# Performance work log

Hardware: AMD Instinct MI355X
Metric: run time of the kernel (lower is better)

The kernel has to match this reference:

```python
import jax, jax.numpy as jnp
import numpy as np
from jax import lax

B, NK, NQ, DK, DV, H = 4, 4096, 4096, 64, 64, 256


def _linear_params(key, fan_in, fan_out):
    kw, kb = jax.random.split(key)
    lim = 1.0 / np.sqrt(fan_in)
    w = jax.random.uniform(kw, (fan_out, fan_in), jnp.float32, -lim, lim)
    b = jax.random.uniform(kb, (fan_out,), jnp.float32, -lim, lim)
    return w, b


def setup_inputs() -> dict:
    key = jax.random.key(0)
    ks = jax.random.split(key, 9)
    inp = {
        "KEY": jax.random.normal(ks[0], (B, NK, DK), jnp.float32),
        "VALUE": jax.random.normal(ks[1], (B, NK, DV), jnp.float32),
        "QUERY": jax.random.normal(ks[2], (B, NQ, DK), jnp.float32),
    }
    inp["W1_w"], inp["W1_b"] = _linear_params(ks[3], DK, H)
    inp["W2_w"], inp["W2_b"] = _linear_params(ks[4], H, H)
    inp["W3_w"], inp["W3_b"] = _linear_params(ks[5], H, DK)
    inp["Wo1_w"], inp["Wo1_b"] = _linear_params(ks[6], DK, H)
    inp["Wo2_w"], inp["Wo2_b"] = _linear_params(ks[7], H, H)
    inp["Wo3_w"], inp["Wo3_b"] = _linear_params(ks[8], H, DV)
    return inp


def _mlp(x, w1, b1, w2, b2, w3, b3):
    h = jax.nn.relu(jnp.einsum('bnd,hd->bnh', x, w1) + b1)
    h = jax.nn.relu(jnp.einsum('bnh,gh->bng', h, w2) + b2)
    return jnp.einsum('bng,og->bno', h, w3) + b3


def _l1_cdist(K, Q):
    # K: [b,nk,d], Q: [b,nq,d] -> [b,nk,nq]; scan over feature dim to avoid
    # materializing the [b,nk,nq,d] difference tensor.
    b, nk, _ = K.shape
    nq = Q.shape[1]

    def body(acc, kq):
        k, q = kq  # [b,nk], [b,nq]
        return acc + jnp.abs(k[:, :, None] - q[:, None, :]), None

    init = jnp.zeros((b, nk, nq), K.dtype)
    score, _ = lax.scan(body, init, (jnp.moveaxis(K, -1, 0), jnp.moveaxis(Q, -1, 0)))
    return score


def reference(KEY, VALUE, QUERY, W1_w, W1_b, W2_w, W2_b, W3_w, W3_b,
              Wo1_w, Wo1_b, Wo2_w, Wo2_b, Wo3_w, Wo3_b):
    Wk = _mlp(KEY, W1_w, W1_b, W2_w, W2_b, W3_w, W3_b)
    Wq = _mlp(QUERY, W1_w, W1_b, W2_w, W2_b, W3_w, W3_b)
    Wo = _mlp(QUERY, Wo1_w, Wo1_b, Wo2_w, Wo2_b, Wo3_w, Wo3_b)
    KEY_scale = KEY * Wk          # [b,nk,dk]
    QUERY_scale = QUERY * Wq      # [b,nq,dk]
    score = _l1_cdist(KEY_scale, QUERY_scale)            # [b,nk,nq]
    attn = jax.nn.softmax(-(score * score) * 0.5, axis=1)  # softmax over keys
    context = jnp.einsum('bik,bij->bkj', attn, VALUE)    # [b,nq,dv]
    # dropout is identity in eval mode
    return context * Wo
```

## Files before the change

kernel.cpp:

```cpp
#include <hip/hip_runtime.h>
#include <hip/hip_bf16.h>
#include <stdint.h>

#define B_DIM 4
#define NKK 4096
#define NQQ 4096
#define DD 64
#define HH 256

typedef __attribute__((ext_vector_type(4))) float floatx4;
typedef __attribute__((ext_vector_type(2))) float floatx2;
typedef __attribute__((ext_vector_type(8))) short bf16x8;

__device__ __forceinline__ float fexp2(float x) { return __builtin_amdgcn_exp2f(x); }
__device__ __forceinline__ unsigned fbits(float x) { return __float_as_uint(x); }
__device__ __forceinline__ float bf2f(unsigned short u) { return __uint_as_float(((unsigned)u) << 16); }

__device__ __forceinline__ floatx2 pk_sub(floatx2 a, floatx2 b) {
  floatx2 d;
  asm("v_pk_add_f32 %0, %1, %2 neg_lo:[0,1] neg_hi:[0,1]" : "=v"(d) : "v"(a), "v"(b));
  return d;
}

__device__ __forceinline__ void splitbf(float x, unsigned short& h, unsigned short& l) {
  unsigned u = fbits(x);
  unsigned hu = (u + 0x7fff + ((u >> 16) & 1)) & 0xffff0000u;
  h = (unsigned short)(hu >> 16);
  l = (unsigned short)(fbits(x - __uint_as_float(hu)) >> 16);
}

#define FSTRIDE 68
#define FSTRIDE4 17

__global__ __launch_bounds__(256) void wsplit_kernel(
    const float* __restrict__ W1a, const float* __restrict__ W2a, const float* __restrict__ W3a,
    const float* __restrict__ W1b, const float* __restrict__ W2b, const float* __restrict__ W3b,
    unsigned short* __restrict__ sp)
{
  int idx = blockIdx.x * 256 + threadIdx.x;
  const int set = idx >= 98304;
  int r = idx - set * 98304;
  unsigned short* base = sp + (size_t)set * 196608;
  const float* src;
  unsigned short *dh, *dl;
  int j;
  if (r < 16384)      { src = set ? W1b : W1a; dh = base;          dl = base + 16384;  j = r; }
  else if (r < 81920) { src = set ? W2b : W2a; dh = base + 32768;  dl = base + 98304;  j = r - 16384; }
  else                { src = set ? W3b : W3a; dh = base + 163840; dl = base + 180224; j = r - 81920; }
  unsigned short h, l;
  splitbf(src[j], h, l);
  dh[j] = h; dl[j] = l;
}

__global__ __launch_bounds__(256) void vtrans_kernel(
    const float* __restrict__ V, unsigned short* __restrict__ Vt)
{
  __shared__ unsigned short t[64][80];
  const int tid = threadIdx.x;
  const int b = blockIdx.y;
  const int k0 = blockIdx.x * 64;
  const float4* V4 = (const float4*)V;
  {
    const int r = tid & 63;
    const int c4 = tid >> 6;
#pragma unroll
    for (int j = 0; j < 4; ++j) {
      float4 f = V4[((size_t)(b * NKK + k0 + r)) * 16 + c4 * 4 + j];
      const int d0 = c4 * 16 + j * 4;
      t[d0 + 0][r] = (unsigned short)(fbits(f.x) >> 16);
      t[d0 + 1][r] = (unsigned short)(fbits(f.y) >> 16);
      t[d0 + 2][r] = (unsigned short)(fbits(f.z) >> 16);
      t[d0 + 3][r] = (unsigned short)(fbits(f.w) >> 16);
    }
  }
  __syncthreads();
  {
    const int d = tid >> 2;
    const int kc = tid & 3;
    uint4 u0 = *(const uint4*)&t[d][kc * 16];
    uint4 u1 = *(const uint4*)&t[d][kc * 16 + 8];
    unsigned short* dst = Vt + ((size_t)(b * 64 + d)) * NKK + k0 + kc * 16;
    *(uint4*)dst = u0;
    *(uint4*)(dst + 8) = u1;
  }
}

#define HSTRIDE 264
__global__ __launch_bounds__(512, 1) void mlpmm_kernel(
    const float* __restrict__ KEY, const float* __restrict__ QUERY,
    const float* __restrict__ B1a, const float* __restrict__ B2a, const float* __restrict__ B3a,
    const float* __restrict__ B1b, const float* __restrict__ B2b, const float* __restrict__ B3b,
    const unsigned short* __restrict__ sp,
    float* __restrict__ Ks, float* __restrict__ Qs, float* __restrict__ Wo)
{
  __shared__ unsigned short Xh[64][72], Xl[64][72];
  __shared__ unsigned short Hsh[64][HSTRIDE], Hsl[64][HSTRIDE];
  const int tid = threadIdx.x;
  const int w = tid >> 6;
  const int lane = tid & 63;
  const int l15 = lane & 15;
  const int quad = lane >> 4;

  const int g = blockIdx.x;
  const float* X;
  float* outp;
  int mulx, t0;
  const unsigned short* wb;
  const float *b1, *b2, *b3;
  if (g < 256)      { X = KEY;   outp = Ks; mulx = 1; t0 = g * 64;         wb = sp;          b1 = B1a; b2 = B2a; b3 = B3a; }
  else if (g < 512) { X = QUERY; outp = Qs; mulx = 1; t0 = (g - 256) * 64; wb = sp;          b1 = B1a; b2 = B2a; b3 = B3a; }
  else              { X = QUERY; outp = Wo; mulx = 0; t0 = (g - 512) * 64; wb = sp + 196608; b1 = B1b; b2 = B2b; b3 = B3b; }
  const unsigned short* W1h = wb;
  const unsigned short* W1l = wb + 16384;
  const unsigned short* W2h = wb + 32768;
  const unsigned short* W2l = wb + 98304;
  const unsigned short* W3h = wb + 163840;
  const unsigned short* W3l = wb + 180224;

  {
    const int t = tid >> 3;
    const int c = (tid & 7) * 8;
    float4 a = *(const float4*)&X[(size_t)(t0 + t) * 64 + c];
    float4 b = *(const float4*)&X[(size_t)(t0 + t) * 64 + c + 4];
    float v[8] = {a.x, a.y, a.z, a.w, b.x, b.y, b.z, b.w};
    unsigned short hs[8], ls[8];
#pragma unroll
    for (int e = 0; e < 8; ++e) splitbf(v[e], hs[e], ls[e]);
    uint4 uh = make_uint4(hs[0] | ((unsigned)hs[1] << 16), hs[2] | ((unsigned)hs[3] << 16),
                          hs[4] | ((unsigned)hs[5] << 16), hs[6] | ((unsigned)hs[7] << 16));
    uint4 ul = make_uint4(ls[0] | ((unsigned)ls[1] << 16), ls[2] | ((unsigned)ls[3] << 16),
                          ls[4] | ((unsigned)ls[5] << 16), ls[6] | ((unsigned)ls[7] << 16));
    *(uint4*)&Xh[t][c] = uh;
    *(uint4*)&Xl[t][c] = ul;
  }
  __syncthreads();

  {
    floatx4 acc[4][2];
#pragma unroll
    for (int nb = 0; nb < 2; ++nb) {
      const float bias = b1[(w * 2 + nb) * 16 + l15];
#pragma unroll
      for (int mb = 0; mb < 4; ++mb) acc[mb][nb] = (floatx4){bias, bias, bias, bias};
    }
#pragma unroll
    for (int kb = 0; kb < 2; ++kb) {
      bf16x8 Ah[4], Al[4];
#pragma unroll
      for (int mb = 0; mb < 4; ++mb) {
        Ah[mb] = *(const bf16x8*)&Xh[mb * 16 + l15][kb * 32 + quad * 8];
        Al[mb] = *(const bf16x8*)&Xl[mb * 16 + l15][kb * 32 + quad * 8];
      }
#pragma unroll
      for (int nb = 0; nb < 2; ++nb) {
        const int n0 = (w * 2 + nb) * 16;
        bf16x8 Bh = *(const bf16x8*)&W1h[(size_t)(n0 + l15) * 64 + kb * 32 + quad * 8];
        bf16x8 Bl = *(const bf16x8*)&W1l[(size_t)(n0 + l15) * 64 + kb * 32 + quad * 8];
#pragma unroll
        for (int mb = 0; mb < 4; ++mb) {
          acc[mb][nb] = __builtin_amdgcn_mfma_f32_16x16x32_bf16(Ah[mb], Bh, acc[mb][nb], 0, 0, 0);
          acc[mb][nb] = __builtin_amdgcn_mfma_f32_16x16x32_bf16(Al[mb], Bh, acc[mb][nb], 0, 0, 0);
          acc[mb][nb] = __builtin_amdgcn_mfma_f32_16x16x32_bf16(Ah[mb], Bl, acc[mb][nb], 0, 0, 0);
        }
      }
    }
#pragma unroll
    for (int mb = 0; mb < 4; ++mb)
#pragma unroll
      for (int nb = 0; nb < 2; ++nb) {
        const int col = (w * 2 + nb) * 16 + l15;
#pragma unroll
        for (int r = 0; r < 4; ++r) {
          const int row = mb * 16 + quad * 4 + r;
          float v = fmaxf(acc[mb][nb][r], 0.0f);
          unsigned short h, l;
          splitbf(v, h, l);
          Hsh[row][col] = h;
          Hsl[row][col] = l;
        }
      }
  }
  __syncthreads();

  {
    floatx4 acc2[4][2];
#pragma unroll
    for (int nb = 0; nb < 2; ++nb) {
      const float bias = b2[(w * 2 + nb) * 16 + l15];
#pragma unroll
      for (int mb = 0; mb < 4; ++mb) acc2[mb][nb] = (floatx4){bias, bias, bias, bias};
    }
#pragma unroll
    for (int kb = 0; kb < 8; ++kb) {
      bf16x8 Ah[4], Al[4];
#pragma unroll
      for (int mb = 0; mb < 4; ++mb) {
        Ah[mb] = *(const bf16x8*)&Hsh[mb * 16 + l15][kb * 32 + quad * 8];
        Al[mb] = *(const bf16x8*)&Hsl[mb * 16 + l15][kb * 32 + quad * 8];
      }
#pragma unroll
      for (int nb = 0; nb < 2; ++nb) {
        const int n0 = (w * 2 + nb) * 16;
        bf16x8 Bh = *(const bf16x8*)&W2h[(size_t)(n0 + l15) * 256 + kb * 32 + quad * 8];
        bf16x8 Bl = *(const bf16x8*)&W2l[(size_t)(n0 + l15) * 256 + kb * 32 + quad * 8];
#pragma unroll
        for (int mb = 0; mb < 4; ++mb) {
          acc2[mb][nb] = __builtin_amdgcn_mfma_f32_16x16x32_bf16(Ah[mb], Bh, acc2[mb][nb], 0, 0, 0);
          acc2[mb][nb] = __builtin_amdgcn_mfma_f32_16x16x32_bf16(Al[mb], Bh, acc2[mb][nb], 0, 0, 0);
          acc2[mb][nb] = __builtin_amdgcn_mfma_f32_16x16x32_bf16(Ah[mb], Bl, acc2[mb][nb], 0, 0, 0);
        }
      }
    }
    __syncthreads();
#pragma unroll
    for (int mb = 0; mb < 4; ++mb)
#pragma unroll
      for (int nb = 0; nb < 2; ++nb) {
        const int col = (w * 2 + nb) * 16 + l15;
#pragma unroll
        for (int r = 0; r < 4; ++r) {
          const int row = mb * 16 + quad * 4 + r;
          float v = fmaxf(acc2[mb][nb][r], 0.0f);
          unsigned short h, l;
          splitbf(v, h, l);
          Hsh[row][col] = h;
          Hsl[row][col] = l;
        }
      }
  }
  __syncthreads();

  {
    const int mp = (w >> 2) * 2;
    const int n0 = (w & 3) * 16;
    const float bias = b3[n0 + l15];
    floatx4 acc3[2];
#pragma unroll
    for (int m = 0; m < 2; ++m) acc3[m] = (floatx4){bias, bias, bias, bias};
#pragma unroll
    for (int kb = 0; kb < 8; ++kb) {
      bf16x8 Ah[2], Al[2];
#pragma unroll
      for (int m = 0; m < 2; ++m) {
        Ah[m] = *(const bf16x8*)&Hsh[(mp + m) * 16 + l15][kb * 32 + quad * 8];
        Al[m] = *(const bf16x8*)&Hsl[(mp + m) * 16 + l15][kb * 32 + quad * 8];
      }
      bf16x8 Bh = *(const bf16x8*)&W3h[(size_t)(n0 + l15) * 256 + kb * 32 + quad * 8];
      bf16x8 Bl = *(const bf16x8*)&W3l[(size_t)(n0 + l15) * 256 + kb * 32 + quad * 8];
#pragma unroll
      for (int m = 0; m < 2; ++m) {
        acc3[m] = __builtin_amdgcn_mfma_f32_16x16x32_bf16(Ah[m], Bh, acc3[m], 0, 0, 0);
        acc3[m] = __builtin_amdgcn_mfma_f32_16x16x32_bf16(Al[m], Bh, acc3[m], 0, 0, 0);
        acc3[m] = __builtin_amdgcn_mfma_f32_16x16x32_bf16(Ah[m], Bl, acc3[m], 0, 0, 0);
      }
    }
#pragma unroll
    for (int m = 0; m < 2; ++m)
#pragma unroll
      for (int r = 0; r < 4; ++r) {
        const int row = (mp + m) * 16 + quad * 4 + r;
        const int col = n0 + l15;
        float v = acc3[m][r];
        if (mulx) v *= (bf2f(Xh[row][col]) + bf2f(Xl[row][col]));
        outp[(size_t)(t0 + row) * 64 + col] = v;
      }
  }
}

template <int ITERS, bool PARTIAL>
__global__ __launch_bounds__(256, 3) void attn_kernel(
    const float* __restrict__ Ksg, const float* __restrict__ Qsg,
    const unsigned short* __restrict__ Vtg, const float* __restrict__ Wog,
    float* __restrict__ outp,
    float* __restrict__ Pm, float* __restrict__ Pl, float* __restrict__ PO)
{
  __shared__ float qsA[32 * FSTRIDE];
  __shared__ float ksA[4][32 * FSTRIDE];
  __shared__ unsigned short psB[4][32 * 40];
  __shared__ float abA[4][32];

  const int tid  = threadIdx.x;
  const int w    = tid >> 6;
  const int lane = tid & 63;
  const int lq   = lane >> 3;
  const int lk   = lane & 7;
  const int l15  = lane & 15;
  const int quad = lane >> 4;
  const int b    = blockIdx.y;
  const int qt   = blockIdx.x * 32;

  {
    const int row = tid >> 3;
    const int c0  = (tid & 7) * 2;
    const float4* Q4 = (const float4*)Qsg;
    float4 g0 = Q4[(size_t)(b * NQQ + qt + row) * 16 + c0];
    float4 g1 = Q4[(size_t)(b * NQQ + qt + row) * 16 + c0 + 1];
    *(float4*)&qsA[row * FSTRIDE + c0 * 4]     = g0;
    *(float4*)&qsA[row * FSTRIDE + c0 * 4 + 4] = g1;
  }
  __syncthreads();

  float m_i[4], l_i[4];
  floatx4 acc[2][4];
#pragma unroll
  for (int i = 0; i < 4; ++i) { m_i[i] = -3.0e38f; l_i[i] = 0.0f; }
#pragma unroll
  for (int mb = 0; mb < 2; ++mb)
#pragma unroll
    for (int nb = 0; nb < 4; ++nb)
#pragma unroll
      for (int r = 0; r < 4; ++r) acc[mb][nb][r] = 0.0f;

  const int kstart = (blockIdx.z * 4 + w) * (ITERS * 32);
  const float4* K4 = (const float4*)Ksg;
  const float NEG_HALF_LOG2E = -0.72134752044448170f;

  const int krow = (lane >> 4);
  const int kci  = lane & 15;

  const unsigned short* vg0 = Vtg + ((size_t)b * 64 + l15) * NKK + kstart + quad * 8;

  float4 kpre[8];
  uint4 vtpre[4];
#pragma unroll
  for (int c = 0; c < 8; ++c)
    kpre[c] = K4[(size_t)(b * NKK + kstart + c * 4 + krow) * 16 + kci];
#pragma unroll
  for (int nb = 0; nb < 4; ++nb)
    vtpre[nb] = *(const uint4*)(vg0 + (size_t)nb * 16 * NKK);

  const floatx4* qb = (const floatx4*)&qsA[lq * FSTRIDE];
  const floatx4* kb = (const floatx4*)&ksA[w][lk * FSTRIDE];

  for (int it = 0; it < ITERS; ++it) {
#pragma unroll
    for (int c = 0; c < 8; ++c)
      *(float4*)&ksA[w][(c * 4 + krow) * FSTRIDE + kci * 4] = kpre[c];

    {
      const int itn = (it + 1 < ITERS) ? it + 1 : it;
#pragma unroll
      for (int c = 0; c < 8; ++c)
        kpre[c] = K4[(size_t)(b * NKK + kstart + itn * 32 + c * 4 + krow) * 16 + kci];
    }

    float s[4][4];
#pragma unroll
    for (int i = 0; i < 4; ++i)
#pragma unroll
      for (int j = 0; j < 4; ++j) s[i][j] = 0.0f;

#pragma unroll
    for (int dc = 0; dc < 16; ++dc) {
      floatx4 qv[4], kv[4];
#pragma unroll
      for (int i = 0; i < 4; ++i) qv[i] = qb[i * (8 * FSTRIDE4) + dc];
#pragma unroll
      for (int j = 0; j < 4; ++j) kv[j] = kb[j * (8 * FSTRIDE4) + dc];
#pragma unroll
      for (int i = 0; i < 4; ++i) {
        const floatx2 qlo = qv[i].lo, qhi = qv[i].hi;
#pragma unroll
        for (int j = 0; j < 4; ++j) {
          floatx2 d0 = pk_sub(qlo, kv[j].lo);
          floatx2 d1 = pk_sub(qhi, kv[j].hi);
          s[i][j] += __builtin_fabsf(d0.x);
          s[i][j] += __builtin_fabsf(d0.y);
          s[i][j] += __builtin_fabsf(d1.x);
          s[i][j] += __builtin_fabsf(d1.y);
        }
      }
    }

    float a_row[4];
#pragma unroll
    for (int i = 0; i < 4; ++i) {
      float smin = fminf(fminf(s[i][0], s[i][1]), fminf(s[i][2], s[i][3]));
      smin = fminf(smin, __shfl_xor(smin, 1));
      smin = fminf(smin, __shfl_xor(smin, 2));
      smin = fminf(smin, __shfl_xor(smin, 4));
      const float tmax = smin * smin * NEG_HALF_LOG2E;
      const float mn = fmaxf(m_i[i], tmax);
      a_row[i] = fexp2(m_i[i] - mn);
      m_i[i] = mn;
      float ps = 0.0f;
#pragma unroll
      for (int j = 0; j < 4; ++j) {
        const float sv = s[i][j];
        const float e = fexp2(fmaf(sv * NEG_HALF_LOG2E, sv, -mn));
        ps += e;
        psB[w][(lq + 8 * i) * 40 + lk + 8 * j] = (unsigned short)(fbits(e) >> 16);
      }
      l_i[i] = fmaf(l_i[i], a_row[i], ps);
    }
    if (lk == 0) {
#pragma unroll
      for (int i = 0; i < 4; ++i) abA[w][lq + 8 * i] = a_row[i];
    }

    {
      bf16x8 afrag[2];
#pragma unroll
      for (int mb = 0; mb < 2; ++mb)
        afrag[mb] = *(const bf16x8*)&psB[w][(mb * 16 + l15) * 40 + quad * 8];

      const floatx4 arv0 = *(const floatx4*)&abA[w][quad * 4];
      const floatx4 arv1 = *(const floatx4*)&abA[w][16 + quad * 4];

#pragma unroll
      for (int nb = 0; nb < 4; ++nb) {
        bf16x8 bfrag = __builtin_bit_cast(bf16x8, vtpre[nb]);
        acc[0][nb] *= arv0;
        acc[1][nb] *= arv1;
        acc[0][nb] = __builtin_amdgcn_mfma_f32_16x16x32_bf16(afrag[0], bfrag, acc[0][nb], 0, 0, 0);
        acc[1][nb] = __builtin_amdgcn_mfma_f32_16x16x32_bf16(afrag[1], bfrag, acc[1][nb], 0, 0, 0);
      }
    }

    {
      const int itn = (it + 1 < ITERS) ? it + 1 : it;
#pragma unroll
      for (int nb = 0; nb < 4; ++nb)
        vtpre[nb] = *(const uint4*)(vg0 + (size_t)nb * 16 * NKK + itn * 32);
    }
  }

#pragma unroll
  for (int i = 0; i < 4; ++i) {
    float l = l_i[i];
    l += __shfl_xor(l, 1);
    l += __shfl_xor(l, 2);
    l += __shfl_xor(l, 4);
    l_i[i] = l;
  }
  float* ovl = (float*)&psB[w][0];
  if (lk == 0) {
#pragma unroll
    for (int i = 0; i < 4; ++i) {
      ovl[lq + 8 * i]      = m_i[i];
      ovl[32 + lq + 8 * i] = l_i[i];
    }
  }
#pragma unroll
  for (int mb = 0; mb < 2; ++mb)
#pragma unroll
    for (int nb = 0; nb < 4; ++nb)
#pragma unroll
      for (int r = 0; r < 4; ++r)
        ksA[w][(mb * 16 + quad * 4 + r) * 64 + nb * 16 + l15] = acc[mb][nb][r];
  __syncthreads();

  {
    const int q = tid >> 3;
    const int dbase = (tid & 7) * 8;
    const float m0 = ((const float*)&psB[0][0])[q];
    const float m1 = ((const float*)&psB[1][0])[q];
    const float m2 = ((const float*)&psB[2][0])[q];
    const float m3 = ((const float*)&psB[3][0])[q];
    const float M = fmaxf(fmaxf(m0, m1), fmaxf(m2, m3));
    const float s0 = fexp2(m0 - M), s1 = fexp2(m1 - M);
    const float s2v = fexp2(m2 - M), s3 = fexp2(m3 - M);
    const float L = ((const float*)&psB[0][0])[32 + q] * s0 +
                    ((const float*)&psB[1][0])[32 + q] * s1 +
                    ((const float*)&psB[2][0])[32 + q] * s2v +
                    ((const float*)&psB[3][0])[32 + q] * s3;
    if (PARTIAL) {
      const size_t p = (size_t)(blockIdx.z * 4 + b) * 128 + blockIdx.x;
      if (dbase == 0) { Pm[p * 32 + q] = M; Pl[p * 32 + q] = L; }
      float* dst = PO + p * 2048 + q * 64 + dbase;
#pragma unroll
      for (int c = 0; c < 8; ++c) {
        const int d = dbase + c;
        dst[c] = s0 * ksA[0][q * 64 + d] + s1 * ksA[1][q * 64 + d] +
                 s2v * ksA[2][q * 64 + d] + s3 * ksA[3][q * 64 + d];
      }
    } else {
      const float rL = 1.0f / L;
      const size_t gbase = (size_t)(b * NQQ + qt + q) * 64 + dbase;
#pragma unroll
      for (int c = 0; c < 8; ++c) {
        const int d = dbase + c;
        float o = s0 * ksA[0][q * 64 + d] + s1 * ksA[1][q * 64 + d] +
                  s2v * ksA[2][q * 64 + d] + s3 * ksA[3][q * 64 + d];
        outp[gbase + c] = o * rL * Wog[gbase + c];
      }
    }
  }
}

__global__ __launch_bounds__(256) void amerge_kernel(
    const float* __restrict__ Pm, const float* __restrict__ Pl,
    const float* __restrict__ PO, const float* __restrict__ Wog,
    float* __restrict__ outp)
{
  const int tid = threadIdx.x;
  const int qt = blockIdx.x;
  const int b = blockIdx.y;
  const int q = tid >> 3;
  const int dbase = (tid & 7) * 8;
  const size_t p0 = (size_t)b * 128 + qt;
  const size_t p1 = (size_t)(4 + b) * 128 + qt;
  const float m0 = Pm[p0 * 32 + q], m1 = Pm[p1 * 32 + q];
  const float l0 = Pl[p0 * 32 + q], l1 = Pl[p1 * 32 + q];
  const float M = fmaxf(m0, m1);
  const float w0 = fexp2(m0 - M), w1 = fexp2(m1 - M);
  const float rL = 1.0f / (w0 * l0 + w1 * l1);
  const float* o0 = PO + p0 * 2048 + q * 64 + dbase;
  const float* o1 = PO + p1 * 2048 + q * 64 + dbase;
  const size_t g = ((size_t)b * NQQ + qt * 32 + q) * 64 + dbase;
#pragma unroll
  for (int c = 0; c < 8; ++c)
    outp[g + c] = (w0 * o0[c] + w1 * o1[c]) * rL * Wog[g + c];
}

extern "C" void kernel_launch(void* const* d_in, const int* in_sizes, int n_in,
                              void* d_out, int out_size, void* d_ws, size_t ws_size,
                              hipStream_t stream) {
  (void)in_sizes; (void)n_in; (void)out_size;
  const float* KEY   = (const float*)d_in[0];
  const float* VALUE = (const float*)d_in[1];
  const float* QUERY = (const float*)d_in[2];
  const float* W1w = (const float*)d_in[3];
  const float* W1b = (const float*)d_in[4];
  const float* W2w = (const float*)d_in[5];
  const float* W2b = (const float*)d_in[6];
  const float* W3w = (const float*)d_in[7];
  const float* W3b = (const float*)d_in[8];
  const float* Wo1w = (const float*)d_in[9];
  const float* Wo1b = (const float*)d_in[10];
  const float* Wo2w = (const float*)d_in[11];
  const float* Wo2b = (const float*)d_in[12];
  const float* Wo3w = (const float*)d_in[13];
  const float* Wo3b = (const float*)d_in[14];

  float* ws = (float*)d_ws;
  const size_t tsz = (size_t)B_DIM * NKK * DD;
  float* Ks = ws;
  float* Qs = ws + tsz;
  float* Wo = ws + 2 * tsz;
  unsigned short* Vtg = (unsigned short*)(ws + 3 * tsz);
  unsigned short* sp  = Vtg + tsz;
  float* Pm = ws + 3 * tsz + tsz / 2 + 196608;
  float* Pl = Pm + 32768;
  float* PO = Pl + 32768;
  float* outf = (float*)d_out;

  const size_t ws_need = (size_t)(3 * tsz + tsz / 2 + 196608 + 2 * 32768 + 2097152) * 4;
  const bool partial = ws_size >= ws_need;

  wsplit_kernel<<<dim3(768), 256, 0, stream>>>(W1w, W2w, W3w, Wo1w, Wo2w, Wo3w, sp);
  vtrans_kernel<<<dim3(NKK / 64, B_DIM), 256, 0, stream>>>(VALUE, Vtg);
  mlpmm_kernel<<<dim3(768), 512, 0, stream>>>(
      KEY, QUERY, W1b, W2b, W3b, Wo1b, Wo2b, Wo3b, sp, Ks, Qs, Wo);
  if (partial) {
    attn_kernel<16, true><<<dim3(NQQ / 32, B_DIM, 2), 256, 0, stream>>>(
        Ks, Qs, Vtg, Wo, outf, Pm, Pl, PO);
    amerge_kernel<<<dim3(NQQ / 32, B_DIM), 256, 0, stream>>>(Pm, Pl, PO, Wo, outf);
  } else {
    attn_kernel<32, false><<<dim3(NQQ / 32, B_DIM, 1), 256, 0, stream>>>(
        Ks, Qs, Vtg, Wo, outf, Pm, Pl, PO);
  }
}
```

Measured before the change: 440.5 us.

## Split attention key range three ways with uneven slices and tighter P stride

Raises the split-K factor of the attention kernel from 2 to 3 blocks per query tile. The 12 warp slices get uneven key counts (11 or 10 iterations of 32 keys) to cover all 4096 keys, and the merge kernel combines three partial softmax states. This gives 1536 blocks instead of 1024, which is meant to fill the GPU's compute units more evenly and reduce tail imbalance. The cost is more partial-output traffic and a larger merge, plus runtime loop bounds. The P staging buffer row stride also drops from 40 to 36 shorts, which changes the LDS bank mapping and footprint.

```diff
diff --git a/kernel.cpp b/kernel.cpp
--- a/kernel.cpp
+++ b/kernel.cpp
@@ -31,6 +31,7 @@
 
 #define FSTRIDE 68
 #define FSTRIDE4 17
+#define PSTRIDE 36
 
 __global__ __launch_bounds__(256) void wsplit_kernel(
     const float* __restrict__ W1a, const float* __restrict__ W2a, const float* __restrict__ W3a,
@@ -267,7 +268,7 @@
   }
 }
 
-template <int ITERS, bool PARTIAL>
+template <bool PARTIAL>
 __global__ __launch_bounds__(256, 3) void attn_kernel(
     const float* __restrict__ Ksg, const float* __restrict__ Qsg,
     const unsigned short* __restrict__ Vtg, const float* __restrict__ Wog,
@@ -276,7 +277,7 @@
 {
   __shared__ float qsA[32 * FSTRIDE];
   __shared__ float ksA[4][32 * FSTRIDE];
-  __shared__ unsigned short psB[4][32 * 40];
+  __shared__ unsigned short psB[4][32 * PSTRIDE];
   __shared__ float abA[4][32];
 
   const int tid  = threadIdx.x;
@@ -311,7 +312,15 @@
 #pragma unroll
       for (int r = 0; r < 4; ++r) acc[mb][nb][r] = 0.0f;
 
-  const int kstart = (blockIdx.z * 4 + w) * (ITERS * 32);
+  int kstart, iters;
+  if (PARTIAL) {
+    const int slice = blockIdx.z * 4 + w;
+    iters  = (slice < 8) ? 11 : 10;
+    kstart = (slice < 8) ? slice * 352 : 2816 + (slice - 8) * 320;
+  } else {
+    iters  = 32;
+    kstart = w * 1024;
+  }
   const float4* K4 = (const float4*)Ksg;
   const float NEG_HALF_LOG2E = -0.72134752044448170f;
 
@@ -332,13 +341,13 @@
   const floatx4* qb = (const floatx4*)&qsA[lq * FSTRIDE];
   const floatx4* kb = (const floatx4*)&ksA[w][lk * FSTRIDE];
 
-  for (int it = 0; it < ITERS; ++it) {
+  for (int it = 0; it < iters; ++it) {
 #pragma unroll
     for (int c = 0; c < 8; ++c)
       *(float4*)&ksA[w][(c * 4 + krow) * FSTRIDE + kci * 4] = kpre[c];
 
     {
-      const int itn = (it + 1 < ITERS) ? it + 1 : it;
+      const int itn = (it + 1 < iters) ? it + 1 : it;
 #pragma unroll
       for (int c = 0; c < 8; ++c)
         kpre[c] = K4[(size_t)(b * NKK + kstart + itn * 32 + c * 4 + krow) * 16 + kci];
@@ -389,7 +398,7 @@
         const float sv = s[i][j];
         const float e = fexp2(fmaf(sv * NEG_HALF_LOG2E, sv, -mn));
         ps += e;
-        psB[w][(lq + 8 * i) * 40 + lk + 8 * j] = (unsigned short)(fbits(e) >> 16);
+        psB[w][(lq + 8 * i) * PSTRIDE + lk + 8 * j] = (unsigned short)(fbits(e) >> 16);
       }
       l_i[i] = fmaf(l_i[i], a_row[i], ps);
     }
@@ -402,7 +411,7 @@
       bf16x8 afrag[2];
 #pragma unroll
       for (int mb = 0; mb < 2; ++mb)
-        afrag[mb] = *(const bf16x8*)&psB[w][(mb * 16 + l15) * 40 + quad * 8];
+        afrag[mb] = *(const bf16x8*)&psB[w][(mb * 16 + l15) * PSTRIDE + quad * 8];
 
       const floatx4 arv0 = *(const floatx4*)&abA[w][quad * 4];
       const floatx4 arv1 = *(const floatx4*)&abA[w][16 + quad * 4];
@@ -418,7 +427,7 @@
     }
 
     {
-      const int itn = (it + 1 < ITERS) ? it + 1 : it;
+      const int itn = (it + 1 < iters) ? it + 1 : it;
 #pragma unroll
       for (int nb = 0; nb < 4; ++nb)
         vtpre[nb] = *(const uint4*)(vg0 + (size_t)nb * 16 * NKK + itn * 32);
@@ -498,19 +507,27 @@
   const int b = blockIdx.y;
   const int q = tid >> 3;
   const int dbase = (tid & 7) * 8;
-  const size_t p0 = (size_t)b * 128 + qt;
-  const size_t p1 = (size_t)(4 + b) * 128 + qt;
-  const float m0 = Pm[p0 * 32 + q], m1 = Pm[p1 * 32 + q];
-  const float l0 = Pl[p0 * 32 + q], l1 = Pl[p1 * 32 + q];
-  const float M = fmaxf(m0, m1);
-  const float w0 = fexp2(m0 - M), w1 = fexp2(m1 - M);
-  const float rL = 1.0f / (w0 * l0 + w1 * l1);
-  const float* o0 = PO + p0 * 2048 + q * 64 + dbase;
-  const float* o1 = PO + p1 * 2048 + q * 64 + dbase;
+  size_t p[3];
+  float mv[3], lv[3];
+#pragma unroll
+  for (int s = 0; s < 3; ++s) {
+    p[s] = (size_t)(s * 4 + b) * 128 + qt;
+    mv[s] = Pm[p[s] * 32 + q];
+    lv[s] = Pl[p[s] * 32 + q];
+  }
+  const float M = fmaxf(fmaxf(mv[0], mv[1]), mv[2]);
+  float wsum = 0.0f, wgt[3];
+#pragma unroll
+  for (int s = 0; s < 3; ++s) { wgt[s] = fexp2(mv[s] - M); wsum += wgt[s] * lv[s]; }
+  const float rL = 1.0f / wsum;
   const size_t g = ((size_t)b * NQQ + qt * 32 + q) * 64 + dbase;
 #pragma unroll
-  for (int c = 0; c < 8; ++c)
-    outp[g + c] = (w0 * o0[c] + w1 * o1[c]) * rL * Wog[g + c];
+  for (int c = 0; c < 8; ++c) {
+    float o = 0.0f;
+#pragma unroll
+    for (int s = 0; s < 3; ++s) o += wgt[s] * PO[p[s] * 2048 + q * 64 + dbase + c];
+    outp[g + c] = o * rL * Wog[g + c];
+  }
 }
 
 extern "C" void kernel_launch(void* const* d_in, const int* in_sizes, int n_in,
@@ -541,11 +558,11 @@
   unsigned short* Vtg = (unsigned short*)(ws + 3 * tsz);
   unsigned short* sp  = Vtg + tsz;
   float* Pm = ws + 3 * tsz + tsz / 2 + 196608;
-  float* Pl = Pm + 32768;
-  float* PO = Pl + 32768;
+  float* Pl = Pm + 49152;
+  float* PO = Pl + 49152;
   float* outf = (float*)d_out;
 
-  const size_t ws_need = (size_t)(3 * tsz + tsz / 2 + 196608 + 2 * 32768 + 2097152) * 4;
+  const size_t ws_need = (size_t)(3 * tsz + tsz / 2 + 196608 + 2 * 49152 + 3145728) * 4;
   const bool partial = ws_size >= ws_need;
 
   wsplit_kernel<<<dim3(768), 256, 0, stream>>>(W1w, W2w, W3w, Wo1w, Wo2w, Wo3w, sp);
@@ -553,11 +570,11 @@
   mlpmm_kernel<<<dim3(768), 512, 0, stream>>>(
       KEY, QUERY, W1b, W2b, W3b, Wo1b, Wo2b, Wo3b, sp, Ks, Qs, Wo);
   if (partial) {
-    attn_kernel<16, true><<<dim3(NQQ / 32, B_DIM, 2), 256, 0, stream>>>(
+    attn_kernel<true><<<dim3(NQQ / 32, B_DIM, 3), 256, 0, stream>>>(
         Ks, Qs, Vtg, Wo, outf, Pm, Pl, PO);
     amerge_kernel<<<dim3(NQQ / 32, B_DIM), 256, 0, stream>>>(Pm, Pl, PO, Wo, outf);
   } else {
-    attn_kernel<32, false><<<dim3(NQQ / 32, B_DIM, 1), 256, 0, stream>>>(
+    attn_kernel<false><<<dim3(NQQ / 32, B_DIM, 1), 256, 0, stream>>>(
         Ks, Qs, Vtg, Wo, outf, Pm, Pl, PO);
   }
 }
```

After: 412.6 us. 1.07x faster.
